# Performance work log

Measured on AMD Instinct MI355X. Metric: run time of the kernel, lower is better.

The kernel has to match this reference:

```python
import jax, jax.numpy as jnp
import numpy as np

E = 1024   # embedding_size
H = 16     # num_heads
DH = E // H


def setup_inputs() -> dict:
    key = jax.random.key(0)
    ks = jax.random.split(key, 11)
    B, S = 2, 2048
    std = 0.02
    return {
        "query": jax.random.normal(ks[0], (B, S, E), jnp.float32),
        "key": jax.random.normal(ks[1], (B, S, E), jnp.float32),
        "value": jax.random.normal(ks[2], (B, S, E), jnp.float32),
        "Wq": jax.random.normal(ks[3], (E, E), jnp.float32) * std,
        "bq": jnp.zeros((E,), jnp.float32),
        "Wk": jax.random.normal(ks[4], (E, E), jnp.float32) * std,
        "bk": jnp.zeros((E,), jnp.float32),
        "Wv": jax.random.normal(ks[5], (E, E), jnp.float32) * std,
        "bv": jnp.zeros((E,), jnp.float32),
        "Wo": jax.random.normal(ks[6], (E, E), jnp.float32) * std,
        "bo": jnp.zeros((E,), jnp.float32),
    }


def _split_heads(x, B, S):
    # [B,S,E] -> [B,H,S,DH]
    return x.reshape(B, S, H, DH).transpose(0, 2, 1, 3)


def reference(query, key, value, Wq, bq, Wk, bk, Wv, bv, Wo, bo):
    B, S, _ = query.shape
    # torch Linear: y = x @ W.T + b
    q = _split_heads(query @ Wq.T + bq, B, S)
    k = _split_heads(key @ Wk.T + bk, B, key.shape[1])
    v = _split_heads(value @ Wv.T + bv, B, value.shape[1])
    # naive unscaled attention (original has no 1/sqrt(d) factor)
    scores = jnp.einsum("bhsd,bhtd->bhst", q, k)  # [B,H,S,T]
    attn = jax.nn.softmax(scores, axis=-1)
    out = jnp.einsum("bhst,bhtd->bhsd", attn, v)  # [B,H,S,DH]
    out = out.transpose(0, 2, 1, 3).reshape(B, S, E)
    return out @ Wo.T + bo
```

## Files before the change

kernel.cpp:

```cpp
#include <hip/hip_runtime.h>
#include <hip/hip_bf16.h>

constexpr int kB   = 2;
constexpr int kS   = 2048;
constexpr int kE   = 1024;
constexpr int kH   = 16;
constexpr int kDH  = 64;
constexpr int kTok = kB * kS;

typedef short bf16x8 __attribute__((ext_vector_type(8)));
typedef float f32x4  __attribute__((ext_vector_type(4)));
typedef unsigned short u16x4 __attribute__((ext_vector_type(4)));

__device__ __forceinline__ float bf2f(unsigned short s) {
  union { unsigned int u; float f; } c; c.u = ((unsigned int)s) << 16; return c.f;
}
__device__ __forceinline__ unsigned short f2bf(float f) {
  union { float f; unsigned int u; } c; c.f = f;
  unsigned int u = c.u;
  u += 0x7fffu + ((u >> 16) & 1u);
  return (unsigned short)(u >> 16);
}

__device__ __forceinline__ void gl_lds16(const unsigned short* g, unsigned short* l) {
  __builtin_amdgcn_global_load_lds(
      (const __attribute__((address_space(1))) unsigned int*)g,
      (__attribute__((address_space(3))) unsigned int*)l, 16, 0, 0);
}

__global__ void detect_dtype(const unsigned short* __restrict__ q, int* flag) {
  __shared__ int cnt;
  if (threadIdx.x == 0) cnt = 0;
  __syncthreads();
  int bad = 0;
  for (int i = threadIdx.x; i < 4096; i += 256) {
    unsigned int e = (q[i] >> 7) & 0xFF;
    if (e >= 0xC0) bad++;
  }
  atomicAdd(&cnt, bad);
  __syncthreads();
  if (threadIdx.x == 0) *flag = (cnt > 8) ? 1 : 0;
}

struct Seg { const void* src; unsigned short* dst; unsigned int n; unsigned int blk0; };
struct ConvArgs { Seg s[11]; };

__global__ __launch_bounds__(256) void conv_all(ConvArgs a, const int* __restrict__ flag) {
  const unsigned int bid = blockIdx.x;
  int si = 0;
  #pragma unroll
  for (int i = 1; i < 11; ++i)
    if (bid >= a.s[i].blk0) si = i;
  const Seg sg = a.s[si];
  const int i0 = ((int)(bid - sg.blk0) * 256 + threadIdx.x) * 8;
  if (i0 >= (int)sg.n) return;
  if (*flag) {
    const float* s = (const float*)sg.src + i0;
    f32x4 f0 = *(const f32x4*)(s);
    f32x4 f1 = *(const f32x4*)(s + 4);
    bf16x8 v;
    #pragma unroll
    for (int j = 0; j < 4; ++j) v[j]     = (short)f2bf(f0[j]);
    #pragma unroll
    for (int j = 0; j < 4; ++j) v[j + 4] = (short)f2bf(f1[j]);
    *(bf16x8*)&sg.dst[i0] = v;
  } else {
    *(bf16x8*)&sg.dst[i0] = *(const bf16x8*)((const unsigned short*)sg.src + i0);
  }
}

__device__ __forceinline__ void gemm_core(
    const unsigned short* __restrict__ A,
    const unsigned short* __restrict__ W,
    int Kdim, int bM, int bN,
    unsigned short* As, unsigned short* Ws,
    f32x4 acc[4][4])
{
  const int tid  = threadIdx.x;
  const int lane = tid & 63;
  const int wv   = tid >> 6;
  const int wm   = (wv >> 1) * 64;
  const int wn   = (wv & 1) * 64;
  const int lr   = lane & 15;
  const int kq   = (lane >> 4) * 8;

  const int r0 = tid >> 2;
  const int c0 = (tid & 3) * 8;

  const unsigned short* Ag = A + (size_t)(bM + r0) * Kdim + c0;
  const unsigned short* Wg = W + (size_t)(bN + r0) * Kdim + c0;
  unsigned short* lA = &As[tid * 8];
  unsigned short* lW = &Ws[tid * 8];

  for (int k0 = 0; k0 < Kdim; k0 += 32) {
    gl_lds16(Ag + k0,                      lA);
    gl_lds16(Ag + (size_t)64 * Kdim + k0,  lA + 2048);
    gl_lds16(Wg + k0,                      lW);
    gl_lds16(Wg + (size_t)64 * Kdim + k0,  lW + 2048);
    __syncthreads();

    bf16x8 a[4], b[4];
    #pragma unroll
    for (int i = 0; i < 4; ++i)
      a[i] = *(const bf16x8*)&As[(wm + i * 16 + lr) * 32 + kq];
    #pragma unroll
    for (int i = 0; i < 4; ++i)
      b[i] = *(const bf16x8*)&Ws[(wn + i * 16 + lr) * 32 + kq];
    #pragma unroll
    for (int i = 0; i < 4; ++i)
      #pragma unroll
      for (int j = 0; j < 4; ++j)
        acc[i][j] = __builtin_amdgcn_mfma_f32_16x16x32_bf16(a[i], b[j], acc[i][j], 0, 0, 0);
    __syncthreads();
  }
}

__global__ __launch_bounds__(256) void gemm_qkv(
    const unsigned short* __restrict__ Abase,
    const unsigned short* __restrict__ Wbase,
    const unsigned short* __restrict__ biasbase,
    unsigned short* __restrict__ Cbase)
{
  __shared__ unsigned short As[128 * 32];
  __shared__ unsigned short Ws[128 * 32];

  const int z = blockIdx.z;
  const unsigned short* A    = Abase    + (size_t)z * (kTok * kE);
  const unsigned short* W    = Wbase    + (size_t)z * (kE * kE);
  const unsigned short* bias = biasbase + (size_t)z * kE;
  unsigned short* C          = Cbase    + (size_t)z * (kTok * kE);

  const int bM = blockIdx.y * 128;
  const int bN = blockIdx.x * 128;

  f32x4 acc[4][4] = {};
  gemm_core(A, W, kE, bM, bN, As, Ws, acc);

  const int lane = threadIdx.x & 63;
  const int wv   = threadIdx.x >> 6;
  const int wm   = (wv >> 1) * 64;
  const int wn   = (wv & 1) * 64;
  const int lr   = lane & 15;
  const int qd   = lane >> 4;

  if (z == 2) {
    #pragma unroll
    for (int j = 0; j < 4; ++j) {
      const int col = bN + wn + j * 16 + lr;
      const float bb = bf2f(bias[col]);
      #pragma unroll
      for (int i = 0; i < 4; ++i) {
        const int tok = bM + wm + i * 16 + qd * 4;
        const int bb_ = tok >> 11;
        const int s   = tok & 2047;
        u16x4 pk;
        #pragma unroll
        for (int r = 0; r < 4; ++r) pk[r] = f2bf(acc[i][j][r] + bb);
        *(u16x4*)&C[(size_t)bb_ * (kE * kS) + (size_t)col * kS + s] = pk;
      }
    }
  } else {
    #pragma unroll
    for (int j = 0; j < 4; ++j) {
      const int col = bN + wn + j * 16 + lr;
      const float bb = bf2f(bias[col]);
      #pragma unroll
      for (int i = 0; i < 4; ++i)
        #pragma unroll
        for (int r = 0; r < 4; ++r) {
          const int row = bM + wm + i * 16 + qd * 4 + r;
          C[(size_t)row * kE + col] = f2bf(acc[i][j][r] + bb);
        }
    }
  }
}

__global__ __launch_bounds__(256) void gemm_out(
    const unsigned short* __restrict__ A,
    const unsigned short* __restrict__ W,
    const unsigned short* __restrict__ bias,
    void* __restrict__ C,
    const int* __restrict__ flag)
{
  __shared__ unsigned short As[128 * 32];
  __shared__ unsigned short Ws[128 * 32];

  const int bM = blockIdx.y * 128;
  const int bN = blockIdx.x * 128;

  f32x4 acc[4][4] = {};
  gemm_core(A, W, kE, bM, bN, As, Ws, acc);

  const int lane = threadIdx.x & 63;
  const int wv   = threadIdx.x >> 6;
  const int wm   = (wv >> 1) * 64;
  const int wn   = (wv & 1) * 64;
  const int lr   = lane & 15;
  const int qd   = lane >> 4;
  if (*flag) {
    float* Cf = (float*)C;
    #pragma unroll
    for (int j = 0; j < 4; ++j) {
      const int col = bN + wn + j * 16 + lr;
      const float bb = bf2f(bias[col]);
      #pragma unroll
      for (int i = 0; i < 4; ++i)
        #pragma unroll
        for (int r = 0; r < 4; ++r) {
          const int row = bM + wm + i * 16 + qd * 4 + r;
          Cf[(size_t)row * kE + col] = acc[i][j][r] + bb;
        }
    }
  } else {
    unsigned short* Cb = (unsigned short*)C;
    #pragma unroll
    for (int j = 0; j < 4; ++j) {
      const int col = bN + wn + j * 16 + lr;
      const float bb = bf2f(bias[col]);
      #pragma unroll
      for (int i = 0; i < 4; ++i)
        #pragma unroll
        for (int r = 0; r < 4; ++r) {
          const int row = bM + wm + i * 16 + qd * 4 + r;
          Cb[(size_t)row * kE + col] = f2bf(acc[i][j][r] + bb);
        }
    }
  }
}

__global__ __launch_bounds__(256) void attn(
    const unsigned short* __restrict__ Qb,
    const unsigned short* __restrict__ Kb,
    const unsigned short* __restrict__ Vt,
    unsigned short* __restrict__ Ob)
{
  __shared__ unsigned short Qs[64 * 72];
  __shared__ unsigned short Ks[64 * 72];
  __shared__ unsigned short Vs[64 * 72];
  __shared__ unsigned short Ps[64 * 72];

  const int tid  = threadIdx.x;
  const int lane = tid & 63;
  const int w    = tid >> 6;
  const int lr   = lane & 15;
  const int quad = lane >> 4;
  const int kq   = quad * 8;

  const int bh = blockIdx.y;
  const int b  = bh >> 4;
  const int h  = bh & 15;
  const int q0 = blockIdx.x * 64;

  const size_t rowbase = (size_t)b * kS * kE;
  const int hcol = h * kDH;
  const unsigned short* Vbase = Vt + (size_t)b * (kE * kS) + (size_t)hcol * kS;

  #pragma unroll
  for (int issue = 0; issue < 2; ++issue) {
    int g = issue * 256 + tid;
    int r = g >> 3, c = (g & 7) * 8;
    *(bf16x8*)&Qs[r * 72 + c] =
        *(const bf16x8*)&Qb[rowbase + (size_t)(q0 + r) * kE + hcol + c];
  }
  __syncthreads();

  const bf16x8 aq0 = *(const bf16x8*)&Qs[(w * 16 + lr) * 72 + 0 + kq];
  const bf16x8 aq1 = *(const bf16x8*)&Qs[(w * 16 + lr) * 72 + 32 + kq];

  f32x4 o[4] = {};
  float l_r[4] = {0.f, 0.f, 0.f, 0.f};

  for (int t0 = 0; t0 < kS; t0 += 64) {
    __syncthreads();

    #pragma unroll
    for (int issue = 0; issue < 2; ++issue) {
      int g = issue * 256 + tid;
      int r = g >> 3, c = (g & 7) * 8;
      *(bf16x8*)&Ks[r * 72 + c] =
          *(const bf16x8*)&Kb[rowbase + (size_t)(t0 + r) * kE + hcol + c];
      *(bf16x8*)&Vs[r * 72 + c] =
          *(const bf16x8*)&Vbase[(size_t)r * kS + t0 + c];
    }
    __syncthreads();

    f32x4 s[4] = {};
    #pragma unroll
    for (int tn = 0; tn < 4; ++tn) {
      const bf16x8 bk0 = *(const bf16x8*)&Ks[(tn * 16 + lr) * 72 + 0 + kq];
      const bf16x8 bk1 = *(const bf16x8*)&Ks[(tn * 16 + lr) * 72 + 32 + kq];
      s[tn] = __builtin_amdgcn_mfma_f32_16x16x32_bf16(aq0, bk0, s[tn], 0, 0, 0);
      s[tn] = __builtin_amdgcn_mfma_f32_16x16x32_bf16(aq1, bk1, s[tn], 0, 0, 0);
    }

    #pragma unroll
    for (int tn = 0; tn < 4; ++tn)
      #pragma unroll
      for (int r = 0; r < 4; ++r) {
        const float p = __expf(s[tn][r]);
        l_r[r] += p;
        Ps[(w * 16 + quad * 4 + r) * 72 + tn * 16 + lr] = f2bf(p);
      }

    #pragma unroll
    for (int kk = 0; kk < 2; ++kk) {
      const bf16x8 ap = *(const bf16x8*)&Ps[(w * 16 + lr) * 72 + kk * 32 + kq];
      #pragma unroll
      for (int dt = 0; dt < 4; ++dt) {
        const bf16x8 bv = *(const bf16x8*)&Vs[(dt * 16 + lr) * 72 + kk * 32 + kq];
        o[dt] = __builtin_amdgcn_mfma_f32_16x16x32_bf16(ap, bv, o[dt], 0, 0, 0);
      }
    }
  }

  #pragma unroll
  for (int r = 0; r < 4; ++r) {
    #pragma unroll
    for (int off = 1; off < 16; off <<= 1)
      l_r[r] += __shfl_xor(l_r[r], off, 64);
  }

  #pragma unroll
  for (int dt = 0; dt < 4; ++dt) {
    #pragma unroll
    for (int r = 0; r < 4; ++r) {
      const int row = q0 + w * 16 + quad * 4 + r;
      const int col = hcol + dt * 16 + lr;
      Ob[rowbase + (size_t)row * kE + col] = f2bf(o[dt][r] / l_r[r]);
    }
  }
}

extern "C" void kernel_launch(void* const* d_in, const int* in_sizes, int n_in,
                              void* d_out, int out_size, void* d_ws, size_t ws_size,
                              hipStream_t stream) {
  const int nQKV = kTok * kE;
  const int nW   = kE * kE;
  const int nB   = kE;

  char* wsb = (char*)d_ws;
  int* flag = (int*)wsb;
  unsigned short* qc  = (unsigned short*)(wsb + 16);
  unsigned short* kc  = qc  + (size_t)nQKV;
  unsigned short* vc  = kc  + (size_t)nQKV;
  unsigned short* Wqc = vc  + (size_t)nQKV;
  unsigned short* Wkc = Wqc + (size_t)nW;
  unsigned short* Wvc = Wkc + (size_t)nW;
  unsigned short* Woc = Wvc + (size_t)nW;
  unsigned short* bqc = Woc + (size_t)nW;
  unsigned short* bkc = bqc + nB;
  unsigned short* bvc = bkc + nB;
  unsigned short* boc = bvc + nB;
  unsigned short* Qb  = boc + nB;
  unsigned short* Kb  = Qb  + (size_t)nQKV;
  unsigned short* Vtb = Kb  + (size_t)nQKV;
  unsigned short* Ob  = qc;

  detect_dtype<<<1, 256, 0, stream>>>((const unsigned short*)d_in[0], flag);

  ConvArgs ca;
  const void* srcs[11] = { d_in[0], d_in[1], d_in[2], d_in[3], d_in[4], d_in[5],
                           d_in[6], d_in[7], d_in[8], d_in[9], d_in[10] };
  unsigned short* dsts[11] = { qc, kc, vc, Wqc, bqc, Wkc, bkc, Wvc, bvc, Woc, boc };
  const unsigned int ns[11] = { (unsigned)nQKV, (unsigned)nQKV, (unsigned)nQKV,
                                (unsigned)nW, (unsigned)nB, (unsigned)nW, (unsigned)nB,
                                (unsigned)nW, (unsigned)nB, (unsigned)nW, (unsigned)nB };
  unsigned int blk = 0;
  for (int i = 0; i < 11; ++i) {
    ca.s[i].src = srcs[i]; ca.s[i].dst = dsts[i]; ca.s[i].n = ns[i]; ca.s[i].blk0 = blk;
    blk += (ns[i] + 2047) / 2048;
  }
  conv_all<<<blk, 256, 0, stream>>>(ca, flag);

  dim3 blk256(256);
  dim3 gqkv(kE / 128, kTok / 128, 3);
  gemm_qkv<<<gqkv, blk256, 0, stream>>>(qc, Wqc, bqc, Qb);

  dim3 gattn(kS / 64, kB * kH);
  attn<<<gattn, blk256, 0, stream>>>(Qb, Kb, Vtb, Ob);

  dim3 gout(kE / 128, kTok / 128);
  gemm_out<<<gout, blk256, 0, stream>>>(Ob, Woc, boc, d_out, flag);
}
```

Baseline: 301.7 us.

## Add separate V transpose kernel, register-prefetch K/V tiles, swizzle P in LDS

The QKV GEMM now writes V in row-major layout, and a new vtrans kernel transposes it through swizzled LDS into the transposed buffer. This replaces the scattered strided stores in the GEMM epilogue. The attention loop prefetches the next K/V tile into registers while the current tile is computed, to hide global load latency. The P tile in LDS gets an XOR swizzle to reduce bank conflicts. In exchange there is an extra kernel launch and one more round trip of V through memory.

```diff
diff --git a/kernel.cpp b/kernel.cpp
--- a/kernel.cpp
+++ b/kernel.cpp
@@ -10,7 +10,6 @@
 
 typedef short bf16x8 __attribute__((ext_vector_type(8)));
 typedef float f32x4  __attribute__((ext_vector_type(4)));
-typedef unsigned short u16x4 __attribute__((ext_vector_type(4)));
 
 __device__ __forceinline__ float bf2f(unsigned short s) {
   union { unsigned int u; float f; } c; c.u = ((unsigned int)s) << 16; return c.f;
@@ -142,36 +141,50 @@
   const int wn   = (wv & 1) * 64;
   const int lr   = lane & 15;
   const int qd   = lane >> 4;
-
-  if (z == 2) {
-    #pragma unroll
-    for (int j = 0; j < 4; ++j) {
-      const int col = bN + wn + j * 16 + lr;
-      const float bb = bf2f(bias[col]);
-      #pragma unroll
-      for (int i = 0; i < 4; ++i) {
-        const int tok = bM + wm + i * 16 + qd * 4;
-        const int bb_ = tok >> 11;
-        const int s   = tok & 2047;
-        u16x4 pk;
-        #pragma unroll
-        for (int r = 0; r < 4; ++r) pk[r] = f2bf(acc[i][j][r] + bb);
-        *(u16x4*)&C[(size_t)bb_ * (kE * kS) + (size_t)col * kS + s] = pk;
+  #pragma unroll
+  for (int j = 0; j < 4; ++j) {
+    const int col = bN + wn + j * 16 + lr;
+    const float bb = bf2f(bias[col]);
+    #pragma unroll
+    for (int i = 0; i < 4; ++i)
+      #pragma unroll
+      for (int r = 0; r < 4; ++r) {
+        const int row = bM + wm + i * 16 + qd * 4 + r;
+        C[(size_t)row * kE + col] = f2bf(acc[i][j][r] + bb);
       }
-    }
-  } else {
-    #pragma unroll
-    for (int j = 0; j < 4; ++j) {
-      const int col = bN + wn + j * 16 + lr;
-      const float bb = bf2f(bias[col]);
-      #pragma unroll
-      for (int i = 0; i < 4; ++i)
-        #pragma unroll
-        for (int r = 0; r < 4; ++r) {
-          const int row = bM + wm + i * 16 + qd * 4 + r;
-          C[(size_t)row * kE + col] = f2bf(acc[i][j][r] + bb);
-        }
-    }
+  }
+}
+
+__global__ __launch_bounds__(256) void vtrans(
+    const unsigned short* __restrict__ Vb,
+    unsigned short* __restrict__ Vt)
+{
+  __shared__ unsigned short Lt[64 * 72];
+  const int tid = threadIdx.x;
+  const int bh  = blockIdx.y;
+  const int b   = bh >> 4;
+  const int h   = bh & 15;
+  const int hcol = h * kDH;
+  const int s0  = blockIdx.x * 64;
+
+  #pragma unroll
+  for (int issue = 0; issue < 2; ++issue) {
+    int g = issue * 256 + tid;
+    int r = g >> 3, c = (g & 7) * 8;
+    bf16x8 vv = *(const bf16x8*)&Vb[(size_t)(b * kS + s0 + r) * kE + hcol + c];
+    const int swz = ((((r >> 3) ^ (c >> 3)) & 7) << 3) + (r & 7);
+    #pragma unroll
+    for (int i = 0; i < 8; ++i)
+      Lt[(c + i) * 72 + swz] = (unsigned short)vv[i];
+  }
+  __syncthreads();
+  #pragma unroll
+  for (int issue = 0; issue < 2; ++issue) {
+    int g = issue * 256 + tid;
+    int f = g >> 3, tc = (g & 7) * 8;
+    const int blk = ((tc >> 3) ^ (f >> 3)) & 7;
+    bf16x8 vv = *(const bf16x8*)&Lt[f * 72 + (blk << 3)];
+    *(bf16x8*)&Vt[(size_t)b * (kE * kS) + (size_t)(hcol + f) * kS + s0 + tc] = vv;
   }
 }
 
@@ -255,12 +268,14 @@
   const int hcol = h * kDH;
   const unsigned short* Vbase = Vt + (size_t)b * (kE * kS) + (size_t)hcol * kS;
 
+  const int r0 = tid >> 3;
+  const int c0 = (tid & 7) * 8;
+
   #pragma unroll
   for (int issue = 0; issue < 2; ++issue) {
-    int g = issue * 256 + tid;
-    int r = g >> 3, c = (g & 7) * 8;
-    *(bf16x8*)&Qs[r * 72 + c] =
-        *(const bf16x8*)&Qb[rowbase + (size_t)(q0 + r) * kE + hcol + c];
+    int r = issue * 32 + r0;
+    *(bf16x8*)&Qs[r * 72 + c0] =
+        *(const bf16x8*)&Qb[rowbase + (size_t)(q0 + r) * kE + hcol + c0];
   }
   __syncthreads();
 
@@ -270,19 +285,26 @@
   f32x4 o[4] = {};
   float l_r[4] = {0.f, 0.f, 0.f, 0.f};
 
+  bf16x8 rk0 = *(const bf16x8*)&Kb[rowbase + (size_t)(r0)      * kE + hcol + c0];
+  bf16x8 rk1 = *(const bf16x8*)&Kb[rowbase + (size_t)(r0 + 32) * kE + hcol + c0];
+  bf16x8 rv0 = *(const bf16x8*)&Vbase[(size_t)(r0)      * kS + c0];
+  bf16x8 rv1 = *(const bf16x8*)&Vbase[(size_t)(r0 + 32) * kS + c0];
+
   for (int t0 = 0; t0 < kS; t0 += 64) {
     __syncthreads();
-
-    #pragma unroll
-    for (int issue = 0; issue < 2; ++issue) {
-      int g = issue * 256 + tid;
-      int r = g >> 3, c = (g & 7) * 8;
-      *(bf16x8*)&Ks[r * 72 + c] =
-          *(const bf16x8*)&Kb[rowbase + (size_t)(t0 + r) * kE + hcol + c];
-      *(bf16x8*)&Vs[r * 72 + c] =
-          *(const bf16x8*)&Vbase[(size_t)r * kS + t0 + c];
-    }
+    *(bf16x8*)&Ks[ r0       * 72 + c0] = rk0;
+    *(bf16x8*)&Ks[(r0 + 32) * 72 + c0] = rk1;
+    *(bf16x8*)&Vs[ r0       * 72 + c0] = rv0;
+    *(bf16x8*)&Vs[(r0 + 32) * 72 + c0] = rv1;
     __syncthreads();
+
+    const int t1 = t0 + 64;
+    if (t1 < kS) {
+      rk0 = *(const bf16x8*)&Kb[rowbase + (size_t)(t1 + r0)      * kE + hcol + c0];
+      rk1 = *(const bf16x8*)&Kb[rowbase + (size_t)(t1 + r0 + 32) * kE + hcol + c0];
+      rv0 = *(const bf16x8*)&Vbase[(size_t)(r0)      * kS + t1 + c0];
+      rv1 = *(const bf16x8*)&Vbase[(size_t)(r0 + 32) * kS + t1 + c0];
+    }
 
     f32x4 s[4] = {};
     #pragma unroll
@@ -299,12 +321,15 @@
       for (int r = 0; r < 4; ++r) {
         const float p = __expf(s[tn][r]);
         l_r[r] += p;
-        Ps[(w * 16 + quad * 4 + r) * 72 + tn * 16 + lr] = f2bf(p);
+        Ps[(w * 16 + quad * 4 + r) * 72 + ((tn ^ quad) << 4) + lr] = f2bf(p);
       }
 
     #pragma unroll
     for (int kk = 0; kk < 2; ++kk) {
-      const bf16x8 ap = *(const bf16x8*)&Ps[(w * 16 + lr) * 72 + kk * 32 + kq];
+      const int tnr = kk * 2 + (quad >> 1);
+      const int tph = tnr ^ ((lr >> 2) & 3);
+      const bf16x8 ap =
+          *(const bf16x8*)&Ps[(w * 16 + lr) * 72 + (tph << 4) + ((quad & 1) << 3)];
       #pragma unroll
       for (int dt = 0; dt < 4; ++dt) {
         const bf16x8 bv = *(const bf16x8*)&Vs[(dt * 16 + lr) * 72 + kk * 32 + kq];
@@ -353,7 +378,8 @@
   unsigned short* boc = bvc + nB;
   unsigned short* Qb  = boc + nB;
   unsigned short* Kb  = Qb  + (size_t)nQKV;
-  unsigned short* Vtb = Kb  + (size_t)nQKV;
+  unsigned short* Vb  = Kb  + (size_t)nQKV;
+  unsigned short* Vtb = kc;
   unsigned short* Ob  = qc;
 
   detect_dtype<<<1, 256, 0, stream>>>((const unsigned short*)d_in[0], flag);
@@ -376,6 +402,9 @@
   dim3 gqkv(kE / 128, kTok / 128, 3);
   gemm_qkv<<<gqkv, blk256, 0, stream>>>(qc, Wqc, bqc, Qb);
 
+  dim3 gvt(kS / 64, kB * kH);
+  vtrans<<<gvt, blk256, 0, stream>>>(Vb, Vtb);
+
   dim3 gattn(kS / 64, kB * kH);
   attn<<<gattn, blk256, 0, stream>>>(Qb, Kb, Vtb, Ob);
 
```

Measured after the change: 281.8 us. 6.6% less time.
